# Performance work log

Measured on AMD Instinct MI355X. Metric: run time of the kernel, lower is better.

## Reference

```python
import jax, jax.numpy as jnp
import numpy as np

N_NODES = 50000
N_EDGES = 800000
IN_DIM = 128
HID = 256
OUT_DIM = 256
N_HEADS = 8
E_DIM = 64
KV_IN = 2 * IN_DIM + E_DIM  # 320


def _mlp_params(key, din, dhid, dout):
    k1, k2 = jax.random.split(key)
    s1 = 1.0 / np.sqrt(din)
    s2 = 1.0 / np.sqrt(dhid)
    return (jax.random.uniform(k1, (din, dhid), jnp.float32, -s1, s1),
            jnp.zeros((dhid,), jnp.float32),
            jax.random.uniform(k2, (dhid, dout), jnp.float32, -s2, s2),
            jnp.zeros((dout,), jnp.float32))


def setup_inputs() -> dict:
    key = jax.random.key(0)
    kh, ke, kidx, kk, kv, kq = jax.random.split(key, 6)
    h = jax.random.normal(kh, (N_NODES, IN_DIM), jnp.float32)
    e = jax.random.normal(ke, (N_EDGES, E_DIM), jnp.float32)
    edge_index = jax.random.randint(kidx, (2, N_EDGES), 0, N_NODES, jnp.int64)
    Wk1, bk1, Wk2, bk2 = _mlp_params(kk, KV_IN, HID, OUT_DIM)
    Wv1, bv1, Wv2, bv2 = _mlp_params(kv, KV_IN, HID, OUT_DIM)
    Wq1, bq1, Wq2, bq2 = _mlp_params(kq, IN_DIM, HID, OUT_DIM)
    return {"h": h, "e": e, "edge_index": edge_index,
            "Wk1": Wk1, "bk1": bk1, "Wk2": Wk2, "bk2": bk2,
            "Wv1": Wv1, "bv1": bv1, "Wv2": Wv2, "bv2": bv2,
            "Wq1": Wq1, "bq1": bq1, "Wq2": Wq2, "bq2": bq2}


def _mlp(x, W1, b1, W2, b2):
    # MLP(in, out, hidden, norm=False): Linear -> ReLU -> Linear
    return jax.nn.relu(x @ W1 + b1) @ W2 + b2


def reference(h, e, edge_index,
              Wk1, bk1, Wk2, bk2,
              Wv1, bv1, Wv2, bv2,
              Wq1, bq1, Wq2, bq2):
    N = h.shape[0]
    d_head = OUT_DIM // N_HEADS
    src, dst = edge_index[0], edge_index[1]
    # gather endpoints: hi = h[dst], hj = h[src]
    kv_input = jnp.concatenate([e, h[dst], h[src]], axis=-1)  # [E, KV_IN]
    k = _mlp(kv_input, Wk1, bk1, Wk2, bk2).reshape(-1, N_HEADS, d_head)
    v = _mlp(kv_input, Wv1, bv1, Wv2, bv2).reshape(-1, N_HEADS, d_head)
    q = _mlp(h, Wq1, bq1, Wq2, bq2).reshape(-1, N_HEADS, d_head)
    # per-edge logits, scaled dot product [E, H]
    logits = jnp.sum(q[dst] * k, axis=-1) * (1.0 / np.sqrt(d_head))
    # scatter softmax over destination groups
    mx = jax.ops.segment_max(logits, dst, num_segments=N)  # [N, H]
    ex = jnp.exp(logits - mx[dst])
    den = jax.ops.segment_sum(ex, dst, num_segments=N)  # [N, H]
    alpha = ex / den[dst]  # [E, H]
    # weighted scatter-sum aggregate
    m = alpha[..., None] * v  # [E, H, d_head]
    out = jax.ops.segment_sum(m, dst, num_segments=N)  # [N, H, d_head]
    return out.reshape(N, OUT_DIM)
```

## Files before the change

kernel.cpp:

```cpp
#include <hip/hip_runtime.h>

#define NND 50000
#define NE  800000
#define IND 128
#define HD  256
#define OD  256
#define NH  8
#define ED  64

typedef __attribute__((ext_vector_type(8))) short bf16x8;
typedef __attribute__((ext_vector_type(4))) float f32x4;

__device__ __forceinline__ float bf2f(unsigned short u) {
    union { unsigned int i; float f; } x; x.i = ((unsigned int)u) << 16; return x.f;
}
__device__ __forceinline__ unsigned short f2bf(float f) {
    union { float f; unsigned int i; } x; x.f = f;
    unsigned int u = x.i;
    u += 0x7FFFu + ((u >> 16) & 1u);
    return (unsigned short)(u >> 16);
}
__device__ __forceinline__ unsigned int pk2(float a, float b) {
    unsigned int r;
    asm("v_cvt_pk_bf16_f32 %0, %1, %2" : "=v"(r) : "v"(a), "v"(b));
    return r;
}

__global__ void k_hist(const int* __restrict__ eidx, int* __restrict__ cnt) {
    int e = blockIdx.x * 256 + threadIdx.x;
    if (e < NE) atomicAdd(&cnt[eidx[NE + e]], 1);
}

__global__ __launch_bounds__(1024) void k_scan(const int* __restrict__ cnt,
                                               int* __restrict__ head) {
    __shared__ int part[1024];
    const int t = threadIdx.x;
    const int CH = (NND + 1023) / 1024;
    int base = t * CH;
    int s = 0;
    for (int i = 0; i < CH; ++i) { int idx = base + i; if (idx < NND) s += cnt[idx]; }
    part[t] = s;
    __syncthreads();
    for (int off = 1; off < 1024; off <<= 1) {
        int v = (t >= off) ? part[t - off] : 0;
        __syncthreads();
        part[t] += v;
        __syncthreads();
    }
    int excl = (t == 0) ? 0 : part[t - 1];
    for (int i = 0; i < CH; ++i) {
        int idx = base + i; if (idx >= NND) break;
        head[idx] = excl;
        excl += cnt[idx];
    }
}

__global__ void k_scatter(const int* __restrict__ eidx, int* __restrict__ head,
                          int* __restrict__ perm, int* __restrict__ srcS,
                          int* __restrict__ dstS) {
    int e = blockIdx.x * 256 + threadIdx.x;
    if (e < NE) {
        int s = eidx[e];
        int d = eidx[NE + e];
        int pos = atomicAdd(&head[d], 1);
        perm[pos] = e;
        srcS[pos] = s;
        dstS[pos] = d;
    }
}

__global__ void k_packw(const float* __restrict__ W, unsigned short* __restrict__ P,
                        int K, int N, int rowoff) {
    int tid = blockIdx.x * 256 + threadIdx.x;
    if (tid >= K * N) return;
    int j = tid & 7;
    int l = (tid >> 3) & 63;
    int rest = tid >> 9;
    int KS = K >> 5;
    int ks = rest % KS;
    int ct = rest / KS;
    int n = ct * 16 + (l & 15);
    int k = ks * 32 + (l >> 4) * 8 + j;
    P[tid] = f2bf(W[(size_t)(rowoff + k) * N + n]);
}

__device__ __forceinline__ void zero_acc(f32x4 (&acc)[4][4]) {
    #pragma unroll
    for (int c = 0; c < 4; ++c)
        #pragma unroll
        for (int i = 0; i < 4; ++i)
            #pragma unroll
            for (int r = 0; r < 4; ++r) acc[c][i][r] = 0.f;
}

template<int KS, int STRIDE>
__device__ __forceinline__ void gemmT(const unsigned short* X,
                                      const unsigned short* __restrict__ Wp,
                                      int w, int l, f32x4 (&acc)[4][4]) {
    for (int ks = 0; ks < KS; ++ks) {
        bf16x8 wf[4], xf[4];
        #pragma unroll
        for (int c = 0; c < 4; ++c)
            wf[c] = *(const bf16x8*)(Wp + (((4 * w + c) * KS + ks) * 64 + l) * 8);
        #pragma unroll
        for (int i = 0; i < 4; ++i)
            xf[i] = *(const bf16x8*)(X + (i * 16 + (l & 15)) * STRIDE + ks * 32 + (l >> 4) * 8);
        #pragma unroll
        for (int c = 0; c < 4; ++c)
            #pragma unroll
            for (int i = 0; i < 4; ++i)
                acc[c][i] = __builtin_amdgcn_mfma_f32_16x16x32_bf16(wf[c], xf[i], acc[c][i], 0, 0, 0);
    }
}

__device__ __forceinline__ void lin_epi(const unsigned short* __restrict__ Wp,
                                        unsigned short* __restrict__ outp,
                                        const unsigned short* sXp,
                                        int w, int l, int g, int el, int m0) {
    f32x4 acc[4][4];
    zero_acc(acc);
    gemmT<4, 144>(sXp, Wp, w, l, acc);
    #pragma unroll
    for (int c = 0; c < 4; ++c) {
        int hid0 = 64 * w + 16 * c + 4 * g;
        #pragma unroll
        for (int i = 0; i < 4; ++i) {
            int node = m0 + 16 * i + el;
            if (node < NND) {
                uint2 pk;
                pk.x = pk2(acc[c][i][0], acc[c][i][1]);
                pk.y = pk2(acc[c][i][2], acc[c][i][3]);
                *(uint2*)(outp + (size_t)node * HD + hid0) = pk;
            }
        }
    }
}

__global__ __launch_bounds__(256) void k_node(
    const float* __restrict__ h,
    const unsigned short* __restrict__ Wq1p, const float* __restrict__ bq1,
    const unsigned short* __restrict__ Wq2p, const float* __restrict__ bq2,
    unsigned short* __restrict__ qb,
    const unsigned short* __restrict__ WdK, const unsigned short* __restrict__ WsK,
    const unsigned short* __restrict__ WdV, const unsigned short* __restrict__ WsV,
    unsigned short* __restrict__ udK, unsigned short* __restrict__ usK,
    unsigned short* __restrict__ udV, unsigned short* __restrict__ usV)
{
    __shared__ unsigned short sX[64][144];
    __shared__ unsigned short sH[64][272];
    const int t = threadIdx.x, w = t >> 6, l = t & 63;
    const int g = l >> 4, el = l & 15;
    const int m0 = blockIdx.x * 64;

    for (int c = t; c < 2048; c += 256) {
        int row = c >> 5, j = c & 31;
        int node = m0 + row; if (node >= NND) node = NND - 1;
        float4 v = *(const float4*)(h + (size_t)node * IND + j * 4);
        uint2 pk; pk.x = pk2(v.x, v.y); pk.y = pk2(v.z, v.w);
        *(uint2*)(&sX[row][j * 4]) = pk;
    }
    __syncthreads();

    f32x4 acc[4][4];
    zero_acc(acc);
    gemmT<4, 144>(&sX[0][0], Wq1p, w, l, acc);
    #pragma unroll
    for (int c = 0; c < 4; ++c) {
        int hid0 = 64 * w + 16 * c + 4 * g;
        float4 bv = *(const float4*)(bq1 + hid0);
        #pragma unroll
        for (int i = 0; i < 4; ++i) {
            uint2 pk;
            pk.x = pk2(fmaxf(acc[c][i][0] + bv.x, 0.f), fmaxf(acc[c][i][1] + bv.y, 0.f));
            pk.y = pk2(fmaxf(acc[c][i][2] + bv.z, 0.f), fmaxf(acc[c][i][3] + bv.w, 0.f));
            *(uint2*)(&sH[16 * i + el][hid0]) = pk;
        }
    }
    __syncthreads();

    zero_acc(acc);
    gemmT<8, 272>(&sH[0][0], Wq2p, w, l, acc);
    #pragma unroll
    for (int c = 0; c < 4; ++c) {
        int out0 = 64 * w + 16 * c + 4 * g;
        float4 bv = *(const float4*)(bq2 + out0);
        #pragma unroll
        for (int i = 0; i < 4; ++i) {
            int node = m0 + 16 * i + el;
            if (node < NND) {
                uint2 pk;
                pk.x = pk2(acc[c][i][0] + bv.x, acc[c][i][1] + bv.y);
                pk.y = pk2(acc[c][i][2] + bv.z, acc[c][i][3] + bv.w);
                *(uint2*)(qb + (size_t)node * OD + out0) = pk;
            }
        }
    }

    lin_epi(WdK, udK, &sX[0][0], w, l, g, el, m0);
    lin_epi(WsK, usK, &sX[0][0], w, l, g, el, m0);
    lin_epi(WdV, udV, &sX[0][0], w, l, g, el, m0);
    lin_epi(WsV, usV, &sX[0][0], w, l, g, el, m0);
}

struct SmF {
    unsigned short E[64][80];
    unsigned short H[64][272];
    int   Eid[64];
    int   Src[64];
    int   Dst[64];
    float Ex[64][8];
};

__device__ __forceinline__ void epi_pre(SmF& sm, f32x4 (&acc)[4][4],
                                        const float* __restrict__ b1,
                                        int w, int g, int el) {
    #pragma unroll
    for (int c = 0; c < 4; ++c) {
        int hid0 = 64 * w + 16 * c + 4 * g;
        float4 bv = *(const float4*)(b1 + hid0);
        #pragma unroll
        for (int i = 0; i < 4; ++i) {
            uint2 pk;
            pk.x = pk2(acc[c][i][0] + bv.x, acc[c][i][1] + bv.y);
            pk.y = pk2(acc[c][i][2] + bv.z, acc[c][i][3] + bv.w);
            *(uint2*)(&sm.H[16 * i + el][hid0]) = pk;
        }
    }
}

__device__ __forceinline__ void elemwise(SmF& sm,
                                         const unsigned short* __restrict__ ud,
                                         const unsigned short* __restrict__ us,
                                         int t) {
    int er = t >> 2;
    const unsigned short* udr = ud + (size_t)sm.Dst[er] * HD;
    const unsigned short* usr = us + (size_t)sm.Src[er] * HD;
    bf16x8 vd[8], vs[8];
    #pragma unroll
    for (int j = 0; j < 8; ++j) {
        int col = (j * 4 + (t & 3)) * 8;
        vd[j] = *(const bf16x8*)(udr + col);
        vs[j] = *(const bf16x8*)(usr + col);
    }
    #pragma unroll
    for (int j = 0; j < 8; ++j) {
        int col = (j * 4 + (t & 3)) * 8;
        bf16x8 hv = *(const bf16x8*)(&sm.H[er][col]);
        float x[8];
        #pragma unroll
        for (int u = 0; u < 8; ++u) {
            x[u] = bf2f((unsigned short)hv[u]) + bf2f((unsigned short)vd[j][u])
                 + bf2f((unsigned short)vs[j][u]);
            x[u] = fmaxf(x[u], 0.f);
        }
        uint4 o;
        o.x = pk2(x[0], x[1]); o.y = pk2(x[2], x[3]);
        o.z = pk2(x[4], x[5]); o.w = pk2(x[6], x[7]);
        *(uint4*)(&sm.H[er][col]) = o;
    }
}

__global__ __launch_bounds__(256, 3) void k_edgeF(
    const float* __restrict__ eattr,
    const int* __restrict__ perm,
    const int* __restrict__ srcS, const int* __restrict__ dstS,
    const unsigned short* __restrict__ WeK, const float* __restrict__ b1K,
    const unsigned short* __restrict__ W2K, const float* __restrict__ b2K,
    const unsigned short* __restrict__ WeV, const float* __restrict__ b1V,
    const unsigned short* __restrict__ W2V, const float* __restrict__ b2V,
    const unsigned short* __restrict__ udK, const unsigned short* __restrict__ usK,
    const unsigned short* __restrict__ udV, const unsigned short* __restrict__ usV,
    const unsigned short* __restrict__ qb,
    float* __restrict__ den, float* __restrict__ outp)
{
    __shared__ SmF sm;
    const int t = threadIdx.x, w = t >> 6, l = t & 63;
    const int g = l >> 4, el = l & 15;
    const int e0 = blockIdx.x * 64;

    if (t < 64) {
        sm.Eid[t] = perm[e0 + t];
        sm.Src[t] = srcS[e0 + t];
        sm.Dst[t] = dstS[e0 + t];
    }
    __syncthreads();
    for (int c = t; c < 1024; c += 256) {
        int row = c >> 4, j = c & 15;
        float4 v = *(const float4*)(eattr + (size_t)sm.Eid[row] * ED + j * 4);
        uint2 pk; pk.x = pk2(v.x, v.y); pk.y = pk2(v.z, v.w);
        *(uint2*)(&sm.E[row][j * 4]) = pk;
    }
    __syncthreads();

    f32x4 acc[4][4];

    zero_acc(acc);
    gemmT<2, 80>(&sm.E[0][0], WeK, w, l, acc);
    epi_pre(sm, acc, b1K, w, g, el);
    __syncthreads();
    elemwise(sm, udK, usK, t);
    __syncthreads();

    zero_acc(acc);
    gemmT<8, 272>(&sm.H[0][0], W2K, w, l, acc);
    __syncthreads();
    epi_pre(sm, acc, b2K, w, g, el);
    __syncthreads();

    const float scale = 0.17677669529663687f;
    for (int p = t; p < 512; p += 256) {
        int er = p >> 3, hh = p & 7;
        const unsigned short* qrow = qb + (size_t)sm.Dst[er] * OD + hh * 32;
        float s = 0.f;
        #pragma unroll
        for (int jj = 0; jj < 32; jj += 8) {
            bf16x8 qv = *(const bf16x8*)(qrow + jj);
            bf16x8 kv = *(const bf16x8*)(&sm.H[er][hh * 32 + jj]);
            #pragma unroll
            for (int u = 0; u < 8; ++u)
                s += bf2f((unsigned short)qv[u]) * bf2f((unsigned short)kv[u]);
        }
        sm.Ex[er][hh] = __expf(s * scale);
    }
    __syncthreads();
    if (t < NH) {
        float run = 0.f; int prev = sm.Dst[0];
        for (int er = 0; er < 64; ++er) {
            int dn = sm.Dst[er];
            if (dn != prev) { atomicAdd(&den[prev * NH + t], run); run = 0.f; prev = dn; }
            run += sm.Ex[er][t];
        }
        atomicAdd(&den[prev * NH + t], run);
    }
    __syncthreads();

    zero_acc(acc);
    gemmT<2, 80>(&sm.E[0][0], WeV, w, l, acc);
    epi_pre(sm, acc, b1V, w, g, el);
    __syncthreads();
    elemwise(sm, udV, usV, t);
    __syncthreads();

    zero_acc(acc);
    gemmT<8, 272>(&sm.H[0][0], W2V, w, l, acc);
    __syncthreads();

    #pragma unroll
    for (int c = 0; c < 4; ++c) {
        int out0 = 64 * w + 16 * c + 4 * g;
        float4 bv = *(const float4*)(b2V + out0);
        int hh = out0 >> 5;
        #pragma unroll
        for (int i = 0; i < 4; ++i) {
            int edge = 16 * i + el;
            float ex = sm.Ex[edge][hh];
            uint2 pk;
            pk.x = pk2((acc[c][i][0] + bv.x) * ex, (acc[c][i][1] + bv.y) * ex);
            pk.y = pk2((acc[c][i][2] + bv.z) * ex, (acc[c][i][3] + bv.w) * ex);
            *(uint2*)(&sm.H[edge][out0]) = pk;
        }
    }
    __syncthreads();

    {
        float run = 0.f; int prev = sm.Dst[0];
        for (int er = 0; er < 64; ++er) {
            int dn = sm.Dst[er];
            if (dn != prev) {
                atomicAdd(outp + (size_t)prev * OD + t, run);
                run = 0.f; prev = dn;
            }
            run += bf2f(sm.H[er][t]);
        }
        atomicAdd(outp + (size_t)prev * OD + t, run);
    }
}

__global__ void k_norm(float* __restrict__ outp, const float* __restrict__ den) {
    int i = blockIdx.x * 256 + threadIdx.x;
    if (i >= NND * OD / 4) return;
    int node = i >> 6;
    int c4 = i & 63;
    int hh = (c4 >> 3);
    float d = den[node * NH + hh];
    float inv = d > 0.f ? 1.f / d : 0.f;
    float4 v = *(float4*)(outp + (size_t)i * 4);
    v.x *= inv; v.y *= inv; v.z *= inv; v.w *= inv;
    *(float4*)(outp + (size_t)i * 4) = v;
}

extern "C" void kernel_launch(void* const* d_in, const int* in_sizes, int n_in,
                              void* d_out, int out_size, void* d_ws, size_t ws_size,
                              hipStream_t stream)
{
    const float* h   = (const float*)d_in[0];
    const float* e   = (const float*)d_in[1];
    const int*   eid = (const int*)  d_in[2];
    const float* Wk1 = (const float*)d_in[3];
    const float* bk1 = (const float*)d_in[4];
    const float* Wk2 = (const float*)d_in[5];
    const float* bk2 = (const float*)d_in[6];
    const float* Wv1 = (const float*)d_in[7];
    const float* bv1 = (const float*)d_in[8];
    const float* Wv2 = (const float*)d_in[9];
    const float* bv2 = (const float*)d_in[10];
    const float* Wq1 = (const float*)d_in[11];
    const float* bq1 = (const float*)d_in[12];
    const float* Wq2 = (const float*)d_in[13];
    const float* bq2 = (const float*)d_in[14];

    char* ws = (char*)d_ws;
    size_t off = 0;
    auto take = [&](size_t bytes) { char* p = ws + off; off += bytes; return p; };
    unsigned short* qb   = (unsigned short*)take(25600000);
    unsigned short* udK  = (unsigned short*)take(25600000);
    unsigned short* usK  = (unsigned short*)take(25600000);
    unsigned short* udV  = (unsigned short*)take(25600000);
    unsigned short* usV  = (unsigned short*)take(25600000);
    float*          den  = (float*)         take(1600000);
    int*            cnt  = (int*)           take(200000);
    int*            head = (int*)           take(200000);
    int*            perm = (int*)           take(3200000);
    int*            srcS = (int*)           take(3200000);
    int*            dstS = (int*)           take(3200000);
    unsigned short* Wq1p = (unsigned short*)take(65536);
    unsigned short* Wq2p = (unsigned short*)take(131072);
    unsigned short* WeK  = (unsigned short*)take(32768);
    unsigned short* W2K  = (unsigned short*)take(131072);
    unsigned short* WdK  = (unsigned short*)take(65536);
    unsigned short* WsK  = (unsigned short*)take(65536);
    unsigned short* WeV  = (unsigned short*)take(32768);
    unsigned short* W2V  = (unsigned short*)take(131072);
    unsigned short* WdV  = (unsigned short*)take(65536);
    unsigned short* WsV  = (unsigned short*)take(65536);
    const size_t needed = off;
    if (ws_size < needed) return;

    hipMemsetAsync(d_out, 0, (size_t)NND * OD * sizeof(float), stream);
    hipMemsetAsync(den, 0, (size_t)NND * NH * sizeof(float), stream);
    hipMemsetAsync(cnt, 0, (size_t)NND * sizeof(int), stream);

    k_hist<<<(NE + 255) / 256, 256, 0, stream>>>(eid, cnt);
    k_scan<<<1, 1024, 0, stream>>>(cnt, head);
    k_scatter<<<(NE + 255) / 256, 256, 0, stream>>>(eid, head, perm, srcS, dstS);

    k_packw<<<(IND * HD + 255) / 256, 256, 0, stream>>>(Wq1, Wq1p, IND, HD, 0);
    k_packw<<<(HD * OD + 255) / 256, 256, 0, stream>>>(Wq2, Wq2p, HD, OD, 0);
    k_packw<<<(ED * HD + 255) / 256, 256, 0, stream>>>(Wk1, WeK, ED, HD, 0);
    k_packw<<<(HD * OD + 255) / 256, 256, 0, stream>>>(Wk2, W2K, HD, OD, 0);
    k_packw<<<(IND * HD + 255) / 256, 256, 0, stream>>>(Wk1, WdK, IND, HD, 64);
    k_packw<<<(IND * HD + 255) / 256, 256, 0, stream>>>(Wk1, WsK, IND, HD, 192);
    k_packw<<<(ED * HD + 255) / 256, 256, 0, stream>>>(Wv1, WeV, ED, HD, 0);
    k_packw<<<(HD * OD + 255) / 256, 256, 0, stream>>>(Wv2, W2V, HD, OD, 0);
    k_packw<<<(IND * HD + 255) / 256, 256, 0, stream>>>(Wv1, WdV, IND, HD, 64);
    k_packw<<<(IND * HD + 255) / 256, 256, 0, stream>>>(Wv1, WsV, IND, HD, 192);

    k_node<<<(NND + 63) / 64, 256, 0, stream>>>(h, Wq1p, bq1, Wq2p, bq2, qb,
                                                WdK, WsK, WdV, WsV,
                                                udK, usK, udV, usV);

    k_edgeF<<<NE / 64, 256, 0, stream>>>(e, perm, srcS, dstS,
                                         WeK, bk1, W2K, bk2,
                                         WeV, bv1, W2V, bv2,
                                         udK, usK, udV, usV,
                                         qb, den, (float*)d_out);

    k_norm<<<(NND * OD / 4 + 255) / 256, 256, 0, stream>>>((float*)d_out, den);
}
```

Baseline: 861.0 us.

## Load edge features into registers, shrink LDS padding, raise occupancy, merge weight packing

The edge kernel no longer stages the edge attributes in shared memory. Each lane gathers its MFMA operand fragments straight from global memory into registers, and reloads them before the V projection. Shared-memory row padding shrinks (272→264, 144→136), the Eid and E arrays are removed, and launch bounds rise from 3 to 4 blocks per CU so more waves can run at once. The ten weight-packing launches are merged into one kernel. The risks are the extra global reads of e, higher register pressure under the tighter launch bound, and possible LDS bank conflicts from the new strides.

```diff
diff --git a/kernel.cpp b/kernel.cpp
--- a/kernel.cpp
+++ b/kernel.cpp
@@ -69,10 +69,9 @@
     }
 }
 
-__global__ void k_packw(const float* __restrict__ W, unsigned short* __restrict__ P,
-                        int K, int N, int rowoff) {
-    int tid = blockIdx.x * 256 + threadIdx.x;
-    if (tid >= K * N) return;
+__device__ __forceinline__ void pack1(const float* __restrict__ W,
+                                      unsigned short* __restrict__ P,
+                                      int K, int N, int rowoff, int tid) {
     int j = tid & 7;
     int l = (tid >> 3) & 63;
     int rest = tid >> 9;
@@ -84,6 +83,29 @@
     P[tid] = f2bf(W[(size_t)(rowoff + k) * N + n]);
 }
 
+__global__ void k_packall(const float* __restrict__ Wq1, const float* __restrict__ Wq2,
+                          const float* __restrict__ Wk1, const float* __restrict__ Wk2,
+                          const float* __restrict__ Wv1, const float* __restrict__ Wv2,
+                          unsigned short* __restrict__ Wq1p, unsigned short* __restrict__ Wq2p,
+                          unsigned short* __restrict__ WeK,  unsigned short* __restrict__ W2K,
+                          unsigned short* __restrict__ WdK,  unsigned short* __restrict__ WsK,
+                          unsigned short* __restrict__ WeV,  unsigned short* __restrict__ W2V,
+                          unsigned short* __restrict__ WdV,  unsigned short* __restrict__ WsV)
+{
+    int tid = blockIdx.x * 256 + threadIdx.x;
+    int chunk = tid >> 14;
+    if      (chunk < 2)   pack1(Wq1, Wq1p, 128, 256, 0,   tid);
+    else if (chunk < 6)   pack1(Wq2, Wq2p, 256, 256, 0,   tid - (2 << 14));
+    else if (chunk < 7)   pack1(Wk1, WeK,   64, 256, 0,   tid - (6 << 14));
+    else if (chunk < 11)  pack1(Wk2, W2K,  256, 256, 0,   tid - (7 << 14));
+    else if (chunk < 13)  pack1(Wk1, WdK,  128, 256, 64,  tid - (11 << 14));
+    else if (chunk < 15)  pack1(Wk1, WsK,  128, 256, 192, tid - (13 << 14));
+    else if (chunk < 16)  pack1(Wv1, WeV,   64, 256, 0,   tid - (15 << 14));
+    else if (chunk < 20)  pack1(Wv2, W2V,  256, 256, 0,   tid - (16 << 14));
+    else if (chunk < 22)  pack1(Wv1, WdV,  128, 256, 64,  tid - (20 << 14));
+    else                  pack1(Wv1, WsV,  128, 256, 192, tid - (22 << 14));
+}
+
 __device__ __forceinline__ void zero_acc(f32x4 (&acc)[4][4]) {
     #pragma unroll
     for (int c = 0; c < 4; ++c)
@@ -113,13 +135,47 @@
     }
 }
 
+__device__ __forceinline__ void gemmR(const bf16x8 (&ef)[2][4],
+                                      const unsigned short* __restrict__ Wp,
+                                      int w, int l, f32x4 (&acc)[4][4]) {
+    #pragma unroll
+    for (int ks = 0; ks < 2; ++ks) {
+        bf16x8 wf[4];
+        #pragma unroll
+        for (int c = 0; c < 4; ++c)
+            wf[c] = *(const bf16x8*)(Wp + (((4 * w + c) * 2 + ks) * 64 + l) * 8);
+        #pragma unroll
+        for (int c = 0; c < 4; ++c)
+            #pragma unroll
+            for (int i = 0; i < 4; ++i)
+                acc[c][i] = __builtin_amdgcn_mfma_f32_16x16x32_bf16(wf[c], ef[ks][i], acc[c][i], 0, 0, 0);
+    }
+}
+
+__device__ __forceinline__ void loadE(bf16x8 (&ef)[2][4],
+                                      const float* __restrict__ eattr,
+                                      const int (&eids)[4], int g) {
+    #pragma unroll
+    for (int ks = 0; ks < 2; ++ks)
+        #pragma unroll
+        for (int i = 0; i < 4; ++i) {
+            const float* p = eattr + (size_t)eids[i] * ED + ks * 32 + g * 8;
+            float4 a = *(const float4*)p;
+            float4 b = *(const float4*)(p + 4);
+            union { unsigned int u[4]; bf16x8 v; } cv;
+            cv.u[0] = pk2(a.x, a.y); cv.u[1] = pk2(a.z, a.w);
+            cv.u[2] = pk2(b.x, b.y); cv.u[3] = pk2(b.z, b.w);
+            ef[ks][i] = cv.v;
+        }
+}
+
 __device__ __forceinline__ void lin_epi(const unsigned short* __restrict__ Wp,
                                         unsigned short* __restrict__ outp,
                                         const unsigned short* sXp,
                                         int w, int l, int g, int el, int m0) {
     f32x4 acc[4][4];
     zero_acc(acc);
-    gemmT<4, 144>(sXp, Wp, w, l, acc);
+    gemmT<4, 136>(sXp, Wp, w, l, acc);
     #pragma unroll
     for (int c = 0; c < 4; ++c) {
         int hid0 = 64 * w + 16 * c + 4 * g;
@@ -146,8 +202,8 @@
     unsigned short* __restrict__ udK, unsigned short* __restrict__ usK,
     unsigned short* __restrict__ udV, unsigned short* __restrict__ usV)
 {
-    __shared__ unsigned short sX[64][144];
-    __shared__ unsigned short sH[64][272];
+    __shared__ unsigned short sX[64][136];
+    __shared__ unsigned short sH[64][264];
     const int t = threadIdx.x, w = t >> 6, l = t & 63;
     const int g = l >> 4, el = l & 15;
     const int m0 = blockIdx.x * 64;
@@ -163,7 +219,7 @@
 
     f32x4 acc[4][4];
     zero_acc(acc);
-    gemmT<4, 144>(&sX[0][0], Wq1p, w, l, acc);
+    gemmT<4, 136>(&sX[0][0], Wq1p, w, l, acc);
     #pragma unroll
     for (int c = 0; c < 4; ++c) {
         int hid0 = 64 * w + 16 * c + 4 * g;
@@ -179,7 +235,7 @@
     __syncthreads();
 
     zero_acc(acc);
-    gemmT<8, 272>(&sH[0][0], Wq2p, w, l, acc);
+    gemmT<8, 264>(&sH[0][0], Wq2p, w, l, acc);
     #pragma unroll
     for (int c = 0; c < 4; ++c) {
         int out0 = 64 * w + 16 * c + 4 * g;
@@ -203,12 +259,10 @@
 }
 
 struct SmF {
-    unsigned short E[64][80];
-    unsigned short H[64][272];
-    int   Eid[64];
+    unsigned short H[64][264];
     int   Src[64];
     int   Dst[64];
-    float Ex[64][8];
+    float Ex[64][9];
 };
 
 __device__ __forceinline__ void epi_pre(SmF& sm, f32x4 (&acc)[4][4],
@@ -260,7 +314,7 @@
     }
 }
 
-__global__ __launch_bounds__(256, 3) void k_edgeF(
+__global__ __launch_bounds__(256, 4) void k_edgeF(
     const float* __restrict__ eattr,
     const int* __restrict__ perm,
     const int* __restrict__ srcS, const int* __restrict__ dstS,
@@ -279,50 +333,51 @@
     const int e0 = blockIdx.x * 64;
 
     if (t < 64) {
-        sm.Eid[t] = perm[e0 + t];
         sm.Src[t] = srcS[e0 + t];
         sm.Dst[t] = dstS[e0 + t];
     }
-    __syncthreads();
-    for (int c = t; c < 1024; c += 256) {
-        int row = c >> 4, j = c & 15;
-        float4 v = *(const float4*)(eattr + (size_t)sm.Eid[row] * ED + j * 4);
-        uint2 pk; pk.x = pk2(v.x, v.y); pk.y = pk2(v.z, v.w);
-        *(uint2*)(&sm.E[row][j * 4]) = pk;
-    }
+    int eids[4];
+    #pragma unroll
+    for (int i = 0; i < 4; ++i) eids[i] = perm[e0 + 16 * i + el];
+    bf16x8 ef[2][4];
+    loadE(ef, eattr, eids, g);
     __syncthreads();
 
     f32x4 acc[4][4];
 
     zero_acc(acc);
-    gemmT<2, 80>(&sm.E[0][0], WeK, w, l, acc);
+    gemmR(ef, WeK, w, l, acc);
     epi_pre(sm, acc, b1K, w, g, el);
     __syncthreads();
     elemwise(sm, udK, usK, t);
     __syncthreads();
 
     zero_acc(acc);
-    gemmT<8, 272>(&sm.H[0][0], W2K, w, l, acc);
+    gemmT<8, 264>(&sm.H[0][0], W2K, w, l, acc);
     __syncthreads();
     epi_pre(sm, acc, b2K, w, g, el);
     __syncthreads();
 
-    const float scale = 0.17677669529663687f;
-    for (int p = t; p < 512; p += 256) {
-        int er = p >> 3, hh = p & 7;
-        const unsigned short* qrow = qb + (size_t)sm.Dst[er] * OD + hh * 32;
-        float s = 0.f;
-        #pragma unroll
-        for (int jj = 0; jj < 32; jj += 8) {
-            bf16x8 qv = *(const bf16x8*)(qrow + jj);
-            bf16x8 kv = *(const bf16x8*)(&sm.H[er][hh * 32 + jj]);
+    {
+        const float scale = 0.17677669529663687f;
+        #pragma unroll
+        for (int p = t; p < 512; p += 256) {
+            int er = p >> 3, hh = p & 7;
+            const unsigned short* qrow = qb + (size_t)sm.Dst[er] * OD + hh * 32;
+            float s = 0.f;
             #pragma unroll
-            for (int u = 0; u < 8; ++u)
-                s += bf2f((unsigned short)qv[u]) * bf2f((unsigned short)kv[u]);
-        }
-        sm.Ex[er][hh] = __expf(s * scale);
-    }
-    __syncthreads();
+            for (int jj = 0; jj < 32; jj += 8) {
+                bf16x8 qv = *(const bf16x8*)(qrow + jj);
+                bf16x8 kv = *(const bf16x8*)(&sm.H[er][hh * 32 + jj]);
+                #pragma unroll
+                for (int u = 0; u < 8; ++u)
+                    s += bf2f((unsigned short)qv[u]) * bf2f((unsigned short)kv[u]);
+            }
+            sm.Ex[er][hh] = __expf(s * scale);
+        }
+    }
+    __syncthreads();
+
     if (t < NH) {
         float run = 0.f; int prev = sm.Dst[0];
         for (int er = 0; er < 64; ++er) {
@@ -332,17 +387,17 @@
         }
         atomicAdd(&den[prev * NH + t], run);
     }
-    __syncthreads();
-
-    zero_acc(acc);
-    gemmT<2, 80>(&sm.E[0][0], WeV, w, l, acc);
+    loadE(ef, eattr, eids, g);
+    zero_acc(acc);
+    gemmR(ef, WeV, w, l, acc);
+    __syncthreads();
     epi_pre(sm, acc, b1V, w, g, el);
     __syncthreads();
     elemwise(sm, udV, usV, t);
     __syncthreads();
 
     zero_acc(acc);
-    gemmT<8, 272>(&sm.H[0][0], W2V, w, l, acc);
+    gemmT<8, 264>(&sm.H[0][0], W2V, w, l, acc);
     __syncthreads();
 
     #pragma unroll
@@ -444,16 +499,9 @@
     k_scan<<<1, 1024, 0, stream>>>(cnt, head);
     k_scatter<<<(NE + 255) / 256, 256, 0, stream>>>(eid, head, perm, srcS, dstS);
 
-    k_packw<<<(IND * HD + 255) / 256, 256, 0, stream>>>(Wq1, Wq1p, IND, HD, 0);
-    k_packw<<<(HD * OD + 255) / 256, 256, 0, stream>>>(Wq2, Wq2p, HD, OD, 0);
-    k_packw<<<(ED * HD + 255) / 256, 256, 0, stream>>>(Wk1, WeK, ED, HD, 0);
-    k_packw<<<(HD * OD + 255) / 256, 256, 0, stream>>>(Wk2, W2K, HD, OD, 0);
-    k_packw<<<(IND * HD + 255) / 256, 256, 0, stream>>>(Wk1, WdK, IND, HD, 64);
-    k_packw<<<(IND * HD + 255) / 256, 256, 0, stream>>>(Wk1, WsK, IND, HD, 192);
-    k_packw<<<(ED * HD + 255) / 256, 256, 0, stream>>>(Wv1, WeV, ED, HD, 0);
-    k_packw<<<(HD * OD + 255) / 256, 256, 0, stream>>>(Wv2, W2V, HD, OD, 0);
-    k_packw<<<(IND * HD + 255) / 256, 256, 0, stream>>>(Wv1, WdV, IND, HD, 64);
-    k_packw<<<(IND * HD + 255) / 256, 256, 0, stream>>>(Wv1, WsV, IND, HD, 192);
+    k_packall<<<(24 << 14) / 256, 256, 0, stream>>>(Wq1, Wq2, Wk1, Wk2, Wv1, Wv2,
+                                                    Wq1p, Wq2p, WeK, W2K, WdK, WsK,
+                                                    WeV, W2V, WdV, WsV);
 
     k_node<<<(NND + 63) / 64, 256, 0, stream>>>(h, Wq1p, bq1, Wq2p, bq2, qb,
                                                 WdK, WsK, WdV, WsV,
```

Result: slower. 990.9 us (+15.1%).
